# Kernel optimization log

Hardware: AMD Instinct MI355X
Metric: run time of the kernel (lower is better)

The kernel has to match this reference:

```python
import jax, jax.numpy as jnp
import numpy as np
import math

B, C, H, W = 16, 128, 64, 64

def _conv3(x, w, b):
    # 3x3 conv, padding=1 (SAME), NCHW / OIHW
    y = jax.lax.conv_general_dilated(x, w, window_strides=(1, 1), padding='SAME',
                                     dimension_numbers=('NCHW', 'OIHW', 'NCHW'))
    return y + b[None, :, None, None]

def setup_inputs() -> dict:
    key = jax.random.key(0)
    ks = jax.random.split(key, 12)
    s = 0.02
    inp = {
        'F_in': jax.random.normal(ks[0], (B, C, H, W), dtype=jnp.float32),
        'Pspe': jax.random.normal(ks[1], (B, C, C), dtype=jnp.float32),
        'q_w': jax.random.normal(ks[2], (C, C, 3, 3), dtype=jnp.float32) * s,
        'q_b': jnp.zeros((C,), dtype=jnp.float32),
        'k_w': jax.random.normal(ks[3], (C, C, 3, 3), dtype=jnp.float32) * s,
        'k_b': jnp.zeros((C,), dtype=jnp.float32),
        'v_w': jax.random.normal(ks[4], (C, C, 3, 3), dtype=jnp.float32) * s,
        'v_b': jnp.zeros((C,), dtype=jnp.float32),
        'f1_w': jax.random.normal(ks[5], (C, C, 3, 3), dtype=jnp.float32) * s,
        'f1_b': jnp.zeros((C,), dtype=jnp.float32),
        'f2_w': jax.random.normal(ks[6], (C, C, 3, 3), dtype=jnp.float32) * s,
        'f2_b': jnp.zeros((C,), dtype=jnp.float32),
    }
    return inp

def reference(F_in, Pspe, q_w, q_b, k_w, k_b, v_w, v_b, f1_w, f1_b, f2_w, f2_b):
    b, c, h, w = F_in.shape
    hw = h * w
    Qm = _conv3(F_in, q_w, q_b)
    Km = _conv3(F_in, k_w, k_b)
    Vm = _conv3(F_in, v_w, v_b)
    # (B,C,H,W) -> (B,HW,C)
    Q = jnp.transpose(Qm, (0, 2, 3, 1)).reshape(b, hw, c)
    K = jnp.transpose(Km, (0, 2, 3, 1)).reshape(b, hw, c)
    V = jnp.transpose(Vm, (0, 2, 3, 1)).reshape(b, hw, c)
    # channel-wise attention: (B,C,C) = K^T Q, contracting over HW
    attn_logits = jnp.einsum('bnc,bnd->bcd', K, Q) / math.sqrt(hw)
    A = jax.nn.softmax(attn_logits, axis=-1)
    M = jnp.einsum('bce,bed->bcd', Pspe, A)         # prompt fusion
    F3 = jnp.einsum('bnc,bcd->bnd', V, M)           # (B,HW,C)
    F3_map = jnp.transpose(F3.reshape(b, h, w, c), (0, 3, 1, 2))
    # MScanBlock is not defined in the provided source -> identity
    F_ssm = F3_map
    ffn = _conv3(jax.nn.gelu(_conv3(F_ssm, f1_w, f1_b), approximate=False), f2_w, f2_b)
    return F_ssm + ffn
```

## Files before the change

### kernel.cpp

```cpp
#include <hip/hip_runtime.h>
#include <cmath>

typedef unsigned short u16;
typedef __bf16 bf16x8 __attribute__((ext_vector_type(8)));
typedef float f32x4 __attribute__((ext_vector_type(4)));

__device__ __forceinline__ u16 f2bf(float f) {
  unsigned u = __float_as_uint(f);
  u += 0x7fffu + ((u >> 16) & 1u);
  return (u16)(u >> 16);
}
__device__ __forceinline__ float bf2f(u16 h) {
  return __uint_as_float(((unsigned)h) << 16);
}
__device__ __forceinline__ f32x4 mfma_bf16(bf16x8 a, bf16x8 b, f32x4 c) {
  return __builtin_amdgcn_mfma_f32_16x16x32_bf16(a, b, c, 0, 0, 0);
}
__device__ __forceinline__ float gelu_exact(float x) {
  return 0.5f * x * (1.0f + erff(x * 0.70710678118654752440f));
}


__global__ __launch_bounds__(256) void pack_x(const float* __restrict__ Fin,
                                              u16* __restrict__ X) {
  const int b = blockIdx.x >> 6, y = blockIdx.x & 63;
  const int tid = threadIdx.x;
  __shared__ float T[64 * 129];
#pragma unroll
  for (int i = 0; i < 32; ++i) {
    int idx = tid + i * 256;
    int c = idx >> 6, x = idx & 63;
    T[x * 129 + c] = Fin[(size_t)(b * 128 + c) * 4096 + y * 64 + x];
  }
  __syncthreads();
#pragma unroll
  for (int i = 0; i < 4; ++i) {
    int chunk = tid + i * 256;
    int x = chunk >> 4;
    int c0 = (chunk & 15) * 8;
    u16 tmp[8];
#pragma unroll
    for (int e = 0; e < 8; ++e) tmp[e] = f2bf(T[x * 129 + c0 + e]);
    *reinterpret_cast<uint4*>(X + ((size_t)((b * 64 + y) * 64 + x) * 128 + c0)) =
        *reinterpret_cast<const uint4*>(tmp);
  }
}

__global__ __launch_bounds__(256) void pack_w(const float* __restrict__ w0,
                                              const float* __restrict__ w1,
                                              const float* __restrict__ w2,
                                              const float* __restrict__ w3,
                                              const float* __restrict__ w4,
                                              u16* __restrict__ Wpk) {
  int gid = blockIdx.x * 256 + threadIdx.x;
  int lane = gid & 63;
  int nblk = (gid >> 6) & 7;
  int step = (gid >> 9) % 36;
  int conv = gid / (512 * 36);
  if (conv >= 5) return;
  const float* w = conv == 0 ? w0 : conv == 1 ? w1 : conv == 2 ? w2 : conv == 3 ? w3 : w4;
  int tap = step >> 2, cc = step & 3;
  int dy = tap / 3, dx = tap % 3;
  int co = nblk * 16 + (lane & 15);
  int ci0 = cc * 32 + (lane >> 4) * 8;
  u16 tmp[8];
#pragma unroll
  for (int e = 0; e < 8; ++e)
    tmp[e] = f2bf(w[((size_t)(co * 128 + ci0 + e) * 3 + dy) * 3 + dx]);
  size_t off = ((size_t)conv * 36 * 8 * 64 + (size_t)((step * 8 + nblk) * 64 + lane)) * 8;
  *reinterpret_cast<uint4*>(Wpk + off) = *reinterpret_cast<const uint4*>(tmp);
}

template <int MODE>
__global__ __launch_bounds__(256, 2) void conv_gemm(
    const u16* __restrict__ Xin, const u16* __restrict__ Wp,
    const float* __restrict__ bias, u16* __restrict__ OutB,
    float* __restrict__ OutF, const u16* __restrict__ Fssm) {
  __shared__ alignas(16) u16 Xs[4 * 66 * 128];
  const int tid = threadIdx.x;
  const int lane = tid & 63;
  const int wv = tid >> 6;
  const int wm = wv >> 1, wn = wv & 1;
  int mt = blockIdx.x;
  mt = (mt & 7) * 64 + (mt >> 3);
  const int b = mt >> 5;
  const int y0 = (mt & 31) * 2;

#pragma unroll
  for (int i = 0; i < 16; ++i) {
    int j = tid + i * 256;
    int row = j >> 4;
    int c16 = j & 15;
    int ys = row >> 6, x = row & 63;
    int ysrc = y0 - 1 + ys;
    uint4 val = make_uint4(0u, 0u, 0u, 0u);
    if ((unsigned)ysrc < 64u)
      val = *reinterpret_cast<const uint4*>(
          Xin + ((size_t)((b * 64 + ysrc) * 64 + x) * 128 + c16 * 8));
    int xs = x + 1;
    unsigned off = (unsigned)(((ys * 66 + xs) * 128 + c16 * 8) * 2) ^
                   (unsigned)((xs & 7) << 4);
    *reinterpret_cast<uint4*>(reinterpret_cast<char*>(Xs) + off) = val;
  }
  if (tid < 128) {
    int ys = tid >> 5, side = (tid >> 4) & 1, c16 = tid & 15;
    int xs = side ? 65 : 0;
    unsigned off = (unsigned)(((ys * 66 + xs) * 128 + c16 * 8) * 2) ^
                   (unsigned)((xs & 7) << 4);
    *reinterpret_cast<uint4*>(reinterpret_cast<char*>(Xs) + off) =
        make_uint4(0u, 0u, 0u, 0u);
  }
  __syncthreads();

  f32x4 acc[4][4];
#pragma unroll
  for (int i = 0; i < 4; ++i)
#pragma unroll
    for (int j = 0; j < 4; ++j) acc[i][j] = f32x4{0.f, 0.f, 0.f, 0.f};

  const int lm = lane & 15, lq = lane >> 4;
  const u16* wlane = Wp + (size_t)lane * 8;

#pragma unroll
  for (int tap = 0; tap < 9; ++tap) {
    const int dy = tap / 3, dx = tap % 3;
#pragma unroll
    for (int cc = 0; cc < 4; ++cc) {
      const int step = tap * 4 + cc;
      bf16x8 af[4], bfr[4];
#pragma unroll
      for (int i = 0; i < 4; ++i) {
        int pos = wm * 64 + i * 16 + lm;
        int x = pos & 63, yr = pos >> 6;
        int xs = x + dx, ys = yr + dy;
        unsigned off = (unsigned)(((ys * 66 + xs) * 128 + cc * 32 + lq * 8) * 2) ^
                       (unsigned)((xs & 7) << 4);
        af[i] = *reinterpret_cast<const bf16x8*>(
            reinterpret_cast<const char*>(Xs) + off);
      }
#pragma unroll
      for (int j = 0; j < 4; ++j)
        bfr[j] = *reinterpret_cast<const bf16x8*>(
            wlane + (size_t)((step * 8 + wn * 4 + j) * 64) * 8);
#pragma unroll
      for (int i = 0; i < 4; ++i)
#pragma unroll
        for (int j = 0; j < 4; ++j) acc[i][j] = mfma_bf16(af[i], bfr[j], acc[i][j]);
    }
  }

  __syncthreads();

  if (MODE <= 2) {
    u16* T = Xs;
#pragma unroll
    for (int i = 0; i < 4; ++i)
#pragma unroll
      for (int j = 0; j < 4; ++j) {
        int n = wn * 64 + j * 16 + lm;
        float bs = bias[n];
#pragma unroll
        for (int r = 0; r < 4; ++r) {
          int m = wm * 64 + i * 16 + lq * 4 + r;
          float v = acc[i][j][r] + bs;
          if (MODE == 1) v = gelu_exact(v);
          if (MODE == 2)
            T[n * 136 + m] = f2bf(v);
          else
            T[m * 136 + n] = f2bf(v);
        }
      }
    __syncthreads();
    if (MODE == 2) {
      const int ksbase = (mt & 31) * 4;
#pragma unroll
      for (int it = 0; it < 8; ++it) {
        int item = tid + it * 256;
        int l = item & 63, cb = (item >> 6) & 7, ksl = item >> 9;
        int c = cb * 16 + (l & 15);
        int mloc = ksl * 32 + (l >> 4) * 8;
        *reinterpret_cast<uint4*>(
            OutB + (size_t)(((b * 128 + ksbase + ksl) * 8 + cb) * 64 + l) * 8) =
            *reinterpret_cast<const uint4*>(T + c * 136 + mloc);
      }
    } else {
      int rr = tid >> 1, hf = tid & 1;
      const uint4* src = reinterpret_cast<const uint4*>(T + rr * 136 + hf * 64);
      uint4* dst = reinterpret_cast<uint4*>(OutB + ((size_t)(mt * 128 + rr) * 128 + hf * 64));
#pragma unroll
      for (int k = 0; k < 8; ++k) dst[k] = src[k];
    }
  } else {
    float* T = reinterpret_cast<float*>(Xs);
#pragma unroll
    for (int i = 0; i < 4; ++i)
#pragma unroll
      for (int j = 0; j < 4; ++j) {
        int n = wn * 64 + j * 16 + lm;
        float bs = bias[n];
#pragma unroll
        for (int r = 0; r < 4; ++r) {
          int m = wm * 64 + i * 16 + lq * 4 + r;
          float v = acc[i][j][r] + bs + bf2f(Fssm[(size_t)(mt * 128 + m) * 128 + n]);
          T[n * 132 + m] = v;
        }
      }
    __syncthreads();
    int rr = tid >> 1, hf = tid & 1;
    const uint4* src = reinterpret_cast<const uint4*>(T + rr * 132 + hf * 64);
    uint4* dst = reinterpret_cast<uint4*>(
        OutF + ((size_t)(b * 128 + rr) * 4096 + (mt & 31) * 128 + hf * 64));
#pragma unroll
    for (int k = 0; k < 16; ++k) dst[k] = src[k];
  }
}

__global__ __launch_bounds__(256, 2) void attn_s(const u16* __restrict__ QP,
                                                 const u16* __restrict__ KP,
                                                 float* __restrict__ SP) {
  const int tid = threadIdx.x;
  const int lane = tid & 63;
  const int wv = tid >> 6, wm = wv >> 1, wn = wv & 1;
  const int lm = lane & 15, lq = lane >> 4;
  int mt = blockIdx.x;
  mt = (mt & 7) * 32 + (mt >> 3);
  const int b = mt >> 4, sp = mt & 15;

  f32x4 acc[4][4];
#pragma unroll
  for (int i = 0; i < 4; ++i)
#pragma unroll
    for (int j = 0; j < 4; ++j) acc[i][j] = f32x4{0.f, 0.f, 0.f, 0.f};

#pragma unroll
  for (int ksl = 0; ksl < 8; ++ksl) {
    const int ks = sp * 8 + ksl;
    bf16x8 af[4], bfr[4];
#pragma unroll
    for (int i = 0; i < 4; ++i)
      af[i] = *reinterpret_cast<const bf16x8*>(
          KP + (size_t)(((b * 128 + ks) * 8 + wm * 4 + i) * 64 + lane) * 8);
#pragma unroll
    for (int j = 0; j < 4; ++j)
      bfr[j] = *reinterpret_cast<const bf16x8*>(
          QP + (size_t)(((b * 128 + ks) * 8 + wn * 4 + j) * 64 + lane) * 8);
#pragma unroll
    for (int i = 0; i < 4; ++i)
#pragma unroll
      for (int j = 0; j < 4; ++j) acc[i][j] = mfma_bf16(af[i], bfr[j], acc[i][j]);
  }

  float* out = SP + (size_t)(b * 16 + sp) * 16384;
#pragma unroll
  for (int i = 0; i < 4; ++i)
#pragma unroll
    for (int j = 0; j < 4; ++j)
#pragma unroll
      for (int r = 0; r < 4; ++r)
        out[(wm * 64 + i * 16 + lq * 4 + r) * 128 + wn * 64 + j * 16 + lm] =
            acc[i][j][r];
}

__global__ __launch_bounds__(256) void attn_r(const float* __restrict__ SP,
                                              u16* __restrict__ ABP) {
  __shared__ float Sf[32][129];
  __shared__ float Inv[32];
  const int tid = threadIdx.x;
  const int b = blockIdx.x >> 2, eb = blockIdx.x & 3;

#pragma unroll
  for (int it = 0; it < 16; ++it) {
    int id = it * 256 + tid;
    int rl = id >> 7, d = id & 127;
    const float* p = SP + (size_t)b * 16 * 16384 + (size_t)(eb * 32 + rl) * 128 + d;
    float s = 0.f;
#pragma unroll
    for (int sp = 0; sp < 16; ++sp) s += p[(size_t)sp * 16384];
    Sf[rl][d] = s * 0.015625f;
  }
  __syncthreads();

  {
    int rl = tid >> 3, sub = tid & 7;
    float mx = -3.4e38f;
#pragma unroll
    for (int k = 0; k < 16; ++k) mx = fmaxf(mx, Sf[rl][sub + 8 * k]);
    mx = fmaxf(mx, __shfl_xor(mx, 1));
    mx = fmaxf(mx, __shfl_xor(mx, 2));
    mx = fmaxf(mx, __shfl_xor(mx, 4));
    float s = 0.f;
#pragma unroll
    for (int k = 0; k < 16; ++k) {
      float e = __expf(Sf[rl][sub + 8 * k] - mx);
      Sf[rl][sub + 8 * k] = e;
      s += e;
    }
    s += __shfl_xor(s, 1);
    s += __shfl_xor(s, 2);
    s += __shfl_xor(s, 4);
    if (sub == 0) Inv[rl] = 1.0f / s;
  }
  __syncthreads();

#pragma unroll
  for (int it = 0; it < 2; ++it) {
    int item = tid + it * 256;
    int l = item & 63, nb = item >> 6;
    int d = nb * 16 + (l & 15);
    u16 tmp[8];
#pragma unroll
    for (int e = 0; e < 8; ++e) {
      int rloc = (l >> 4) * 8 + e;
      tmp[e] = f2bf(Sf[rloc][d] * Inv[rloc]);
    }
    *reinterpret_cast<uint4*>(ABP + (size_t)(((b * 4 + eb) * 8 + nb) * 64 + l) * 8) =
        *reinterpret_cast<const uint4*>(tmp);
  }
}

__global__ __launch_bounds__(256, 1) void attn_m(const float* __restrict__ Pspe,
                                                 const u16* __restrict__ ABP,
                                                 u16* __restrict__ Mpack) {
  __shared__ u16 Ml[128 * 136];
  const int b = blockIdx.x;
  const int tid = threadIdx.x;
  const int lane = tid & 63;
  const int wv = tid >> 6, wm = wv >> 1, wn = wv & 1;
  const int lm = lane & 15, lq = lane >> 4;

  f32x4 acc[4][4];
#pragma unroll
  for (int i = 0; i < 4; ++i)
#pragma unroll
    for (int j = 0; j < 4; ++j) acc[i][j] = f32x4{0.f, 0.f, 0.f, 0.f};

  const float* P = Pspe + (size_t)b * 128 * 128;
#pragma unroll
  for (int cc = 0; cc < 4; ++cc) {
    int e0 = cc * 32 + lq * 8;
    bf16x8 af[4], bfr[4];
#pragma unroll
    for (int i = 0; i < 4; ++i) {
      const float* p = P + (size_t)(wm * 64 + i * 16 + lm) * 128 + e0;
      union { u16 u[8]; bf16x8 v; } cv;
#pragma unroll
      for (int e = 0; e < 8; ++e) cv.u[e] = f2bf(p[e]);
      af[i] = cv.v;
    }
#pragma unroll
    for (int j = 0; j < 4; ++j)
      bfr[j] = *reinterpret_cast<const bf16x8*>(
          ABP + (size_t)(((b * 4 + cc) * 8 + wn * 4 + j) * 64 + lane) * 8);
#pragma unroll
    for (int i = 0; i < 4; ++i)
#pragma unroll
      for (int j = 0; j < 4; ++j) acc[i][j] = mfma_bf16(af[i], bfr[j], acc[i][j]);
  }

#pragma unroll
  for (int i = 0; i < 4; ++i)
#pragma unroll
    for (int j = 0; j < 4; ++j)
#pragma unroll
      for (int r = 0; r < 4; ++r)
        Ml[(wn * 64 + j * 16 + lm) * 136 + (wm * 64 + i * 16 + lq * 4 + r)] =
            f2bf(acc[i][j][r]);
  __syncthreads();

#pragma unroll
  for (int it = 0; it < 8; ++it) {
    int item = tid + it * 256;
    int l2 = item & 63, nb = (item >> 6) & 7, cc2 = item >> 9;
    int d = nb * 16 + (l2 & 15), c0 = cc2 * 32 + (l2 >> 4) * 8;
    *reinterpret_cast<uint4*>(Mpack + (size_t)b * 16384 + (size_t)item * 8) =
        *reinterpret_cast<const uint4*>(Ml + d * 136 + c0);
  }
}

__global__ __launch_bounds__(256) void f3_gemm(const u16* __restrict__ V,
                                               const u16* __restrict__ Mpack,
                                               u16* __restrict__ Fout) {
  const int tid = threadIdx.x;
  const int lane = tid & 63;
  const int wv = tid >> 6, wm = wv >> 1, wn = wv & 1;
  const int lm = lane & 15, lq = lane >> 4;
  int mt = blockIdx.x;
  mt = (mt & 7) * 64 + (mt >> 3);
  const int b = mt >> 5;

  f32x4 acc[4][4];
#pragma unroll
  for (int i = 0; i < 4; ++i)
#pragma unroll
    for (int j = 0; j < 4; ++j) acc[i][j] = f32x4{0.f, 0.f, 0.f, 0.f};

#pragma unroll
  for (int cc = 0; cc < 4; ++cc) {
    int k0 = cc * 32 + lq * 8;
    bf16x8 af[4], bfr[4];
#pragma unroll
    for (int i = 0; i < 4; ++i)
      af[i] = *reinterpret_cast<const bf16x8*>(
          V + (size_t)(mt * 128 + wm * 64 + i * 16 + lm) * 128 + k0);
#pragma unroll
    for (int j = 0; j < 4; ++j)
      bfr[j] = *reinterpret_cast<const bf16x8*>(
          Mpack + (size_t)b * 16384 + (size_t)((cc * 8 + wn * 4 + j) * 64 + lane) * 8);
#pragma unroll
    for (int i = 0; i < 4; ++i)
#pragma unroll
      for (int j = 0; j < 4; ++j) acc[i][j] = mfma_bf16(af[i], bfr[j], acc[i][j]);
  }

  __shared__ u16 T[128 * 136];
#pragma unroll
  for (int i = 0; i < 4; ++i)
#pragma unroll
    for (int j = 0; j < 4; ++j)
#pragma unroll
      for (int r = 0; r < 4; ++r)
        T[(wm * 64 + i * 16 + lq * 4 + r) * 136 + wn * 64 + j * 16 + lm] =
            f2bf(acc[i][j][r]);
  __syncthreads();
  int rr = tid >> 1, hf = tid & 1;
  const uint4* src = reinterpret_cast<const uint4*>(T + rr * 136 + hf * 64);
  uint4* dst = reinterpret_cast<uint4*>(Fout + ((size_t)(mt * 128 + rr) * 128 + hf * 64));
#pragma unroll
  for (int k = 0; k < 8; ++k) dst[k] = src[k];
}

extern "C" void kernel_launch(void* const* d_in, const int* in_sizes, int n_in,
                              void* d_out, int out_size, void* d_ws, size_t ws_size,
                              hipStream_t stream) {
  const float* F_in = (const float*)d_in[0];
  const float* Pspe = (const float*)d_in[1];
  const float* q_w = (const float*)d_in[2];
  const float* q_b = (const float*)d_in[3];
  const float* k_w = (const float*)d_in[4];
  const float* k_b = (const float*)d_in[5];
  const float* v_w = (const float*)d_in[6];
  const float* v_b = (const float*)d_in[7];
  const float* f1_w = (const float*)d_in[8];
  const float* f1_b = (const float*)d_in[9];
  const float* f2_w = (const float*)d_in[10];
  const float* f2_b = (const float*)d_in[11];
  float* out = (float*)d_out;

  char* ws = (char*)d_ws;
  const size_t SZ = 16777216;
  u16* X = (u16*)(ws);
  u16* QP = (u16*)(ws + SZ);
  u16* KP = (u16*)(ws + 2 * SZ);
  u16* V = (u16*)(ws + 3 * SZ);
  u16* Wpk = (u16*)(ws + 4 * SZ);
  u16* Mpk = (u16*)(ws + 4 * SZ + 1474560);
  float* SP = (float*)ws;
  u16* ABP = KP;
  u16* Fssm = X;
  u16* Hid = QP;

  pack_x<<<1024, 256, 0, stream>>>(F_in, X);
  pack_w<<<360, 256, 0, stream>>>(q_w, k_w, v_w, f1_w, f2_w, Wpk);
  conv_gemm<2><<<512, 256, 0, stream>>>(X, Wpk, q_b, QP, nullptr, nullptr);
  conv_gemm<2><<<512, 256, 0, stream>>>(X, Wpk + 147456, k_b, KP, nullptr, nullptr);
  conv_gemm<0><<<512, 256, 0, stream>>>(X, Wpk + 2 * 147456, v_b, V, nullptr, nullptr);
  attn_s<<<256, 256, 0, stream>>>(QP, KP, SP);
  attn_r<<<64, 256, 0, stream>>>(SP, ABP);
  attn_m<<<16, 256, 0, stream>>>(Pspe, ABP, Mpk);
  f3_gemm<<<512, 256, 0, stream>>>(V, Mpk, Fssm);
  conv_gemm<1><<<512, 256, 0, stream>>>(Fssm, Wpk + 3 * 147456, f1_b, Hid, nullptr, nullptr);
  conv_gemm<3><<<512, 256, 0, stream>>>(Hid, Wpk + 4 * 147456, f2_b, nullptr, out, Fssm);
}
```

Baseline: 199.7 us.

## Fuse Q/K/V convolutions into one kernel sharing the staged input tile

Replaces three separate conv_gemm launches for Q, K and V with a single conv_qkv kernel. It stages the input tile into shared memory once and reuses the A fragments against all three weight sets, with three accumulator sets. This removes two redundant input staging passes and two launches, at the cost of 48 accumulator vectors per thread, which adds register pressure and may lower occupancy under the (256,2) launch bound. It also halves the split-K count in attn_s (128 blocks, 16 k-steps each) so attn_r reduces 8 partials instead of 16, and simplifies the A-offset arithmetic in conv_gemm.

```diff
diff --git a/kernel.cpp b/kernel.cpp
--- a/kernel.cpp
+++ b/kernel.cpp
@@ -71,21 +71,8 @@
   *reinterpret_cast<uint4*>(Wpk + off) = *reinterpret_cast<const uint4*>(tmp);
 }
 
-template <int MODE>
-__global__ __launch_bounds__(256, 2) void conv_gemm(
-    const u16* __restrict__ Xin, const u16* __restrict__ Wp,
-    const float* __restrict__ bias, u16* __restrict__ OutB,
-    float* __restrict__ OutF, const u16* __restrict__ Fssm) {
-  __shared__ alignas(16) u16 Xs[4 * 66 * 128];
-  const int tid = threadIdx.x;
-  const int lane = tid & 63;
-  const int wv = tid >> 6;
-  const int wm = wv >> 1, wn = wv & 1;
-  int mt = blockIdx.x;
-  mt = (mt & 7) * 64 + (mt >> 3);
-  const int b = mt >> 5;
-  const int y0 = (mt & 31) * 2;
-
+__device__ __forceinline__ void stage_tile(const u16* __restrict__ Xin, u16* Xs,
+                                           int tid, int b, int y0) {
 #pragma unroll
   for (int i = 0; i < 16; ++i) {
     int j = tid + i * 256;
@@ -110,6 +97,146 @@
     *reinterpret_cast<uint4*>(reinterpret_cast<char*>(Xs) + off) =
         make_uint4(0u, 0u, 0u, 0u);
   }
+}
+
+__device__ __forceinline__ void epi_pack(f32x4 (&acc)[4][4], const float* __restrict__ bias,
+                                         u16* __restrict__ OutB, u16* T, int tid,
+                                         int wm, int wn, int lm, int lq, int b, int mt) {
+#pragma unroll
+  for (int i = 0; i < 4; ++i)
+#pragma unroll
+    for (int j = 0; j < 4; ++j) {
+      int n = wn * 64 + j * 16 + lm;
+      float bs = bias[n];
+#pragma unroll
+      for (int r = 0; r < 4; ++r) {
+        int m = wm * 64 + i * 16 + lq * 4 + r;
+        T[n * 136 + m] = f2bf(acc[i][j][r] + bs);
+      }
+    }
+  __syncthreads();
+  const int ksbase = (mt & 31) * 4;
+#pragma unroll
+  for (int it = 0; it < 8; ++it) {
+    int item = tid + it * 256;
+    int l = item & 63, cb = (item >> 6) & 7, ksl = item >> 9;
+    int c = cb * 16 + (l & 15);
+    int mloc = ksl * 32 + (l >> 4) * 8;
+    *reinterpret_cast<uint4*>(
+        OutB + (size_t)(((b * 128 + ksbase + ksl) * 8 + cb) * 64 + l) * 8) =
+        *reinterpret_cast<const uint4*>(T + c * 136 + mloc);
+  }
+  __syncthreads();
+}
+
+__device__ __forceinline__ void epi_nat(f32x4 (&acc)[4][4], const float* __restrict__ bias,
+                                        u16* __restrict__ OutB, u16* T, int tid,
+                                        int wm, int wn, int lm, int lq, int mt) {
+#pragma unroll
+  for (int i = 0; i < 4; ++i)
+#pragma unroll
+    for (int j = 0; j < 4; ++j) {
+      int n = wn * 64 + j * 16 + lm;
+      float bs = bias[n];
+#pragma unroll
+      for (int r = 0; r < 4; ++r) {
+        int m = wm * 64 + i * 16 + lq * 4 + r;
+        T[m * 136 + n] = f2bf(acc[i][j][r] + bs);
+      }
+    }
+  __syncthreads();
+  int rr = tid >> 1, hf = tid & 1;
+  const uint4* src = reinterpret_cast<const uint4*>(T + rr * 136 + hf * 64);
+  uint4* dst = reinterpret_cast<uint4*>(OutB + ((size_t)(mt * 128 + rr) * 128 + hf * 64));
+#pragma unroll
+  for (int k = 0; k < 8; ++k) dst[k] = src[k];
+  __syncthreads();
+}
+
+__global__ __launch_bounds__(256, 2) void conv_qkv(
+    const u16* __restrict__ Xin, const u16* __restrict__ Wp,
+    const float* __restrict__ qb, const float* __restrict__ kb,
+    const float* __restrict__ vb, u16* __restrict__ QP,
+    u16* __restrict__ KP, u16* __restrict__ Vout) {
+  __shared__ alignas(16) u16 Xs[4 * 66 * 128];
+  const int tid = threadIdx.x;
+  const int lane = tid & 63;
+  const int wv = tid >> 6;
+  const int wm = wv >> 1, wn = wv & 1;
+  int mt = blockIdx.x;
+  mt = (mt & 7) * 64 + (mt >> 3);
+  const int b = mt >> 5;
+  const int y0 = (mt & 31) * 2;
+
+  stage_tile(Xin, Xs, tid, b, y0);
+  __syncthreads();
+
+  f32x4 acc[3][4][4];
+#pragma unroll
+  for (int c = 0; c < 3; ++c)
+#pragma unroll
+    for (int i = 0; i < 4; ++i)
+#pragma unroll
+      for (int j = 0; j < 4; ++j) acc[c][i][j] = f32x4{0.f, 0.f, 0.f, 0.f};
+
+  const int lm = lane & 15, lq = lane >> 4;
+
+#pragma unroll 1
+  for (int tap = 0; tap < 9; ++tap) {
+    const int dy = (tap * 11) >> 5;
+    const int dx = tap - dy * 3;
+    const int ysrow = (wm + dy) * 66;
+#pragma unroll
+    for (int cc = 0; cc < 4; ++cc) {
+      const int step = tap * 4 + cc;
+      bf16x8 af[4];
+#pragma unroll
+      for (int i = 0; i < 4; ++i) {
+        int xs = i * 16 + lm + dx;
+        unsigned off = (unsigned)(((ysrow + xs) * 128 + cc * 32 + lq * 8) * 2) ^
+                       (unsigned)((xs & 7) << 4);
+        af[i] = *reinterpret_cast<const bf16x8*>(
+            reinterpret_cast<const char*>(Xs) + off);
+      }
+#pragma unroll
+      for (int cv = 0; cv < 3; ++cv) {
+        const u16* wl = Wp + (size_t)cv * 147456 + (size_t)lane * 8;
+        bf16x8 bfr[4];
+#pragma unroll
+        for (int j = 0; j < 4; ++j)
+          bfr[j] = *reinterpret_cast<const bf16x8*>(
+              wl + (size_t)((step * 8 + wn * 4 + j) * 64) * 8);
+#pragma unroll
+        for (int i = 0; i < 4; ++i)
+#pragma unroll
+          for (int j = 0; j < 4; ++j)
+            acc[cv][i][j] = mfma_bf16(af[i], bfr[j], acc[cv][i][j]);
+      }
+    }
+  }
+
+  __syncthreads();
+  epi_pack(acc[0], qb, QP, Xs, tid, wm, wn, lm, lq, b, mt);
+  epi_pack(acc[1], kb, KP, Xs, tid, wm, wn, lm, lq, b, mt);
+  epi_nat(acc[2], vb, Vout, Xs, tid, wm, wn, lm, lq, mt);
+}
+
+template <int MODE>
+__global__ __launch_bounds__(256, 2) void conv_gemm(
+    const u16* __restrict__ Xin, const u16* __restrict__ Wp,
+    const float* __restrict__ bias, u16* __restrict__ OutB,
+    float* __restrict__ OutF, const u16* __restrict__ Fssm) {
+  __shared__ alignas(16) u16 Xs[4 * 66 * 128];
+  const int tid = threadIdx.x;
+  const int lane = tid & 63;
+  const int wv = tid >> 6;
+  const int wm = wv >> 1, wn = wv & 1;
+  int mt = blockIdx.x;
+  mt = (mt & 7) * 64 + (mt >> 3);
+  const int b = mt >> 5;
+  const int y0 = (mt & 31) * 2;
+
+  stage_tile(Xin, Xs, tid, b, y0);
   __syncthreads();
 
   f32x4 acc[4][4];
@@ -124,16 +251,15 @@
 #pragma unroll
   for (int tap = 0; tap < 9; ++tap) {
     const int dy = tap / 3, dx = tap % 3;
+    const int ysrow = (wm + dy) * 66;
 #pragma unroll
     for (int cc = 0; cc < 4; ++cc) {
       const int step = tap * 4 + cc;
       bf16x8 af[4], bfr[4];
 #pragma unroll
       for (int i = 0; i < 4; ++i) {
-        int pos = wm * 64 + i * 16 + lm;
-        int x = pos & 63, yr = pos >> 6;
-        int xs = x + dx, ys = yr + dy;
-        unsigned off = (unsigned)(((ys * 66 + xs) * 128 + cc * 32 + lq * 8) * 2) ^
+        int xs = i * 16 + lm + dx;
+        unsigned off = (unsigned)(((ysrow + xs) * 128 + cc * 32 + lq * 8) * 2) ^
                        (unsigned)((xs & 7) << 4);
         af[i] = *reinterpret_cast<const bf16x8*>(
             reinterpret_cast<const char*>(Xs) + off);
@@ -151,7 +277,7 @@
 
   __syncthreads();
 
-  if (MODE <= 2) {
+  if (MODE == 1) {
     u16* T = Xs;
 #pragma unroll
     for (int i = 0; i < 4; ++i)
@@ -162,34 +288,15 @@
 #pragma unroll
         for (int r = 0; r < 4; ++r) {
           int m = wm * 64 + i * 16 + lq * 4 + r;
-          float v = acc[i][j][r] + bs;
-          if (MODE == 1) v = gelu_exact(v);
-          if (MODE == 2)
-            T[n * 136 + m] = f2bf(v);
-          else
-            T[m * 136 + n] = f2bf(v);
+          T[m * 136 + n] = f2bf(gelu_exact(acc[i][j][r] + bs));
         }
       }
     __syncthreads();
-    if (MODE == 2) {
-      const int ksbase = (mt & 31) * 4;
-#pragma unroll
-      for (int it = 0; it < 8; ++it) {
-        int item = tid + it * 256;
-        int l = item & 63, cb = (item >> 6) & 7, ksl = item >> 9;
-        int c = cb * 16 + (l & 15);
-        int mloc = ksl * 32 + (l >> 4) * 8;
-        *reinterpret_cast<uint4*>(
-            OutB + (size_t)(((b * 128 + ksbase + ksl) * 8 + cb) * 64 + l) * 8) =
-            *reinterpret_cast<const uint4*>(T + c * 136 + mloc);
-      }
-    } else {
-      int rr = tid >> 1, hf = tid & 1;
-      const uint4* src = reinterpret_cast<const uint4*>(T + rr * 136 + hf * 64);
-      uint4* dst = reinterpret_cast<uint4*>(OutB + ((size_t)(mt * 128 + rr) * 128 + hf * 64));
-#pragma unroll
-      for (int k = 0; k < 8; ++k) dst[k] = src[k];
-    }
+    int rr = tid >> 1, hf = tid & 1;
+    const uint4* src = reinterpret_cast<const uint4*>(T + rr * 136 + hf * 64);
+    uint4* dst = reinterpret_cast<uint4*>(OutB + ((size_t)(mt * 128 + rr) * 128 + hf * 64));
+#pragma unroll
+    for (int k = 0; k < 8; ++k) dst[k] = src[k];
   } else {
     float* T = reinterpret_cast<float*>(Xs);
 #pragma unroll
@@ -223,8 +330,8 @@
   const int wv = tid >> 6, wm = wv >> 1, wn = wv & 1;
   const int lm = lane & 15, lq = lane >> 4;
   int mt = blockIdx.x;
-  mt = (mt & 7) * 32 + (mt >> 3);
-  const int b = mt >> 4, sp = mt & 15;
+  mt = (mt & 7) * 16 + (mt >> 3);
+  const int b = mt >> 3, sp = mt & 7;
 
   f32x4 acc[4][4];
 #pragma unroll
@@ -233,8 +340,8 @@
     for (int j = 0; j < 4; ++j) acc[i][j] = f32x4{0.f, 0.f, 0.f, 0.f};
 
 #pragma unroll
-  for (int ksl = 0; ksl < 8; ++ksl) {
-    const int ks = sp * 8 + ksl;
+  for (int ksl = 0; ksl < 16; ++ksl) {
+    const int ks = sp * 16 + ksl;
     bf16x8 af[4], bfr[4];
 #pragma unroll
     for (int i = 0; i < 4; ++i)
@@ -250,7 +357,7 @@
       for (int j = 0; j < 4; ++j) acc[i][j] = mfma_bf16(af[i], bfr[j], acc[i][j]);
   }
 
-  float* out = SP + (size_t)(b * 16 + sp) * 16384;
+  float* out = SP + (size_t)(b * 8 + sp) * 16384;
 #pragma unroll
   for (int i = 0; i < 4; ++i)
 #pragma unroll
@@ -272,10 +379,10 @@
   for (int it = 0; it < 16; ++it) {
     int id = it * 256 + tid;
     int rl = id >> 7, d = id & 127;
-    const float* p = SP + (size_t)b * 16 * 16384 + (size_t)(eb * 32 + rl) * 128 + d;
+    const float* p = SP + (size_t)b * 8 * 16384 + (size_t)(eb * 32 + rl) * 128 + d;
     float s = 0.f;
 #pragma unroll
-    for (int sp = 0; sp < 16; ++sp) s += p[(size_t)sp * 16384];
+    for (int sp = 0; sp < 8; ++sp) s += p[(size_t)sp * 16384];
     Sf[rl][d] = s * 0.015625f;
   }
   __syncthreads();
@@ -461,10 +568,8 @@
 
   pack_x<<<1024, 256, 0, stream>>>(F_in, X);
   pack_w<<<360, 256, 0, stream>>>(q_w, k_w, v_w, f1_w, f2_w, Wpk);
-  conv_gemm<2><<<512, 256, 0, stream>>>(X, Wpk, q_b, QP, nullptr, nullptr);
-  conv_gemm<2><<<512, 256, 0, stream>>>(X, Wpk + 147456, k_b, KP, nullptr, nullptr);
-  conv_gemm<0><<<512, 256, 0, stream>>>(X, Wpk + 2 * 147456, v_b, V, nullptr, nullptr);
-  attn_s<<<256, 256, 0, stream>>>(QP, KP, SP);
+  conv_qkv<<<512, 256, 0, stream>>>(X, Wpk, q_b, k_b, v_b, QP, KP, V);
+  attn_s<<<128, 256, 0, stream>>>(QP, KP, SP);
   attn_r<<<64, 256, 0, stream>>>(SP, ABP);
   attn_m<<<16, 256, 0, stream>>>(Pspe, ABP, Mpk);
   f3_gemm<<<512, 256, 0, stream>>>(V, Mpk, Fssm);
```

Measured after the change: 182.4 us. -8.7%, faster.
